# Kernel optimization log

Measured on AMD Instinct MI355X. Metric: run time of the kernel, lower is better.

The kernel has to match this reference:

```python
import jax, jax.numpy as jnp
import numpy as np

DIM, HEADS, DEPTH, SEQ, LOCAL_W = 1024, 16, 7, 2048, 64
HEAD_DIM = DIM // HEADS
SCALE = 1.0 / HEAD_DIM ** 0.5


def cantor_mask(S, depth, local_window):
    """Allowed (i,j): |i-j| within local window, OR |i-j| lies in the Cantor set
    under `depth` levels of ternary subdivision (no base-3 digit equals 1)."""
    idx = np.arange(S)
    d = np.abs(idx[:, None] - idx[None, :])
    x = d.copy()
    ok = np.ones_like(d, dtype=bool)
    for _ in range(depth):
        ok &= (x % 3) != 1
        x //= 3
    ok &= x == 0  # offset must be < 3**depth
    return jnp.asarray(ok | (d <= local_window))  # [S, S] bool


def setup_inputs() -> dict:
    key = jax.random.key(0)
    ks = jax.random.split(key, 8)
    B = 2
    s = 0.02
    return {
        "query": jax.random.normal(ks[0], (B, SEQ, DIM), jnp.float32),
        "key_value": jax.random.normal(ks[1], (B, SEQ, DIM), jnp.float32),
        "Wq": jax.random.normal(ks[2], (DIM, DIM), jnp.float32) * s,
        "bq": jnp.zeros((DIM,), jnp.float32),
        "Wkv": jax.random.normal(ks[3], (DIM, 2 * DIM), jnp.float32) * s,
        "bkv": jnp.zeros((2 * DIM,), jnp.float32),
        "Wo": jax.random.normal(ks[4], (DIM, DIM), jnp.float32) * s,
        "bo": jnp.zeros((DIM,), jnp.float32),
    }


def reference(query, key_value, Wq, bq, Wkv, bkv, Wo, bo):
    B, S, D = query.shape
    H, hd = HEADS, HEAD_DIM
    mask = cantor_mask(S, DEPTH, LOCAL_W)  # static [S, S] bool

    q = (query @ Wq + bq).reshape(B, S, H, hd).transpose(0, 2, 1, 3)  # [B,H,S,hd]
    kv = (key_value @ Wkv + bkv).reshape(B, S, 2, H, hd).transpose(2, 0, 3, 1, 4)
    k, v = kv[0], kv[1]  # [B,H,S,hd]

    scores = jnp.einsum("bhqd,bhkd->bhqk", q, k) * SCALE
    scores = jnp.where(mask, scores, jnp.finfo(scores.dtype).min)
    attn = jax.nn.softmax(scores, axis=-1)
    out = jnp.einsum("bhqk,bhkd->bhqd", attn, v)  # [B,H,S,hd]
    out = out.transpose(0, 2, 1, 3).reshape(B, S, D)
    return out @ Wo + bo
```

## Files before the change

kernel.cpp:

```cpp
#include <hip/hip_runtime.h>
#include <stdint.h>

typedef _Float16 half_t;
typedef __attribute__((ext_vector_type(8))) _Float16 half8;
typedef __attribute__((ext_vector_type(4))) _Float16 half4;
typedef __attribute__((ext_vector_type(4))) float floatx4;

#define SEQ 2048
#define NH 16
#define HD 64

#define MFMA16(a, b, c) __builtin_amdgcn_mfma_f32_16x16x16f16(a, b, c, 0, 0, 0)
#define MFMA32K(a, b, c) __builtin_amdgcn_mfma_f32_16x16x32_f16(a, b, c, 0, 0, 0)

#define QSCALE 0.1803368801111306f

__global__ __launch_bounds__(256) void prep(
    const float* __restrict__ query, const float* __restrict__ key_value,
    const float* __restrict__ Wq, const float* __restrict__ Wkv,
    const float* __restrict__ Wo, half_t* __restrict__ xq,
    half_t* __restrict__ xkv, half_t* __restrict__ wqT,
    half_t* __restrict__ wkvT, half_t* __restrict__ woT,
    uint8_t* __restrict__ tok, uint8_t* __restrict__ tok16,
    uint64_t* __restrict__ maskw) {
  int bx = blockIdx.x, tid = threadIdx.x;
  if (bx < 2048) {
    const float* s; half_t* d; int base;
    if (bx < 1024) { s = query; d = xq; base = bx * 4096; }
    else { s = key_value; d = xkv; base = (bx - 1024) * 4096; }
#pragma unroll
    for (int u = 0; u < 4; ++u) {
      int i = base + u * 1024 + tid * 4;
      floatx4 v = *(const floatx4*)(s + i);
      half4 h;
      h[0] = (half_t)v[0]; h[1] = (half_t)v[1];
      h[2] = (half_t)v[2]; h[3] = (half_t)v[3];
      *(half4*)(d + i) = h;
    }
    return;
  }
  if (bx < 3072) {
    __shared__ float tile[64][65];
    int id = bx - 2048;
    const float* W; half_t* Wt; int N, nt, kt;
    if (id < 256) { W = Wq; Wt = wqT; N = 1024; nt = id & 15; kt = id >> 4; }
    else if (id < 768) { int i2 = id - 256; W = Wkv; Wt = wkvT; N = 2048; nt = i2 & 31; kt = i2 >> 5; }
    else { int i2 = id - 768; W = Wo; Wt = woT; N = 1024; nt = i2 & 15; kt = i2 >> 4; }
    const int K = 1024;
    int n0 = nt * 64, k0 = kt * 64;
    {
      int rr = tid >> 4, cc = (tid & 15) * 4;
#pragma unroll
      for (int u = 0; u < 4; ++u) {
        floatx4 v = *(const floatx4*)(W + (size_t)(k0 + rr + u * 16) * N + n0 + cc);
        tile[rr + u * 16][cc] = v[0];
        tile[rr + u * 16][cc + 1] = v[1];
        tile[rr + u * 16][cc + 2] = v[2];
        tile[rr + u * 16][cc + 3] = v[3];
      }
    }
    __syncthreads();
    {
      int n = tid >> 2, q4 = tid & 3;
      half_t h[16];
#pragma unroll
      for (int s = 0; s < 16; ++s) h[s] = (half_t)tile[q4 * 16 + s][n];
      half_t* dst = Wt + (size_t)(n0 + n) * K + k0 + q4 * 16;
      *(half8*)dst = *(half8*)&h[0];
      *(half8*)(dst + 8) = *(half8*)&h[8];
    }
    return;
  }
  __shared__ uint8_t slut[2048];
  int ib = bx - 3072;
  for (int d = tid; d < 2048; d += 256) {
    int x = d;
    bool ok = true;
    for (int it = 0; it < 7; ++it) { ok &= ((x % 3) != 1); x /= 3; }
    ok &= (x == 0);
    slut[d] = (ok || d <= 64) ? 1 : 0;
  }
  __syncthreads();
  if (ib == 0) {
    if (tid < 64) {
      int delta = tid - 32;
      int lo = delta * 64 - 63, hi = delta * 64 + 63;
      uint8_t any = 0;
      for (int x = lo; x <= hi; ++x) {
        int a = x < 0 ? -x : x;
        if (a < 2048) any |= slut[a];
      }
      tok[tid] = any;
    }
    {
      int d16 = tid - 128;
      int ctr = d16 * 16;
      uint8_t any = 0;
      for (int x = ctr - 15; x <= ctr + 15; ++x) {
        int a = x < 0 ? -x : x;
        if (a < 2048) any |= slut[a];
      }
      tok16[tid] = any;
    }
  }
  int g = ib * 256 + tid;
  int tt = g - 2048;
  uint64_t w = 0;
  for (int jj = 0; jj < 64; ++jj) {
    int d = tt - jj; d = d < 0 ? -d : d;
    if (d < 2048 && slut[d]) w |= (1ull << jj);
  }
  maskw[g] = w;
}

__device__ __forceinline__ void cp16(half_t* lds, const half_t* g) {
  __builtin_amdgcn_global_load_lds(
      (const __attribute__((address_space(1))) uint32_t*)g,
      (__attribute__((address_space(3))) uint32_t*)lds, 16, 0, 0);
}

__global__ __launch_bounds__(256) void gemm_qkv(
    const half_t* __restrict__ xq, const half_t* __restrict__ xkv,
    const half_t* __restrict__ wqT, const half_t* __restrict__ wkvT,
    const float* __restrict__ bq, const float* __restrict__ bkv,
    half_t* __restrict__ qout, half_t* __restrict__ kout,
    half_t* __restrict__ vTout) {
  extern __shared__ char smemraw[];
  half_t* As = (half_t*)smemraw;
  half_t* Bs = As + 8192;
  const int K = 1024;
  bool isq = blockIdx.y < 8;
  const half_t* A = isq ? xq : xkv;
  const half_t* Bt = isq ? wqT : wkvT;
  const float* bias = isq ? bq : bkv;
  int n0 = (isq ? blockIdx.y : (blockIdx.y - 8)) * 128;
  int m0 = blockIdx.x * 128;

  int tid = threadIdx.x;
  int wave = tid >> 6, lane = tid & 63;
  int c = lane & 15, quad = lane >> 4;
  int wm = (wave >> 1) * 64, wn = (wave & 1) * 64;

  floatx4 acc[4][4] = {};
  int arow = tid >> 2, akc = (tid & 3) * 8;

  cp16(&As[wave * 512], A + (size_t)(m0 + arow) * K + akc);
  cp16(&As[2048 + wave * 512], A + (size_t)(m0 + 64 + arow) * K + akc);
  cp16(&Bs[wave * 512], Bt + (size_t)(n0 + arow) * K + akc);
  cp16(&Bs[2048 + wave * 512], Bt + (size_t)(n0 + 64 + arow) * K + akc);

  for (int kt = 0; kt < 32; ++kt) {
    __syncthreads();
    if (kt + 1 < 32) {
      int k0 = (kt + 1) * 32;
      int b = (kt + 1) & 1;
      cp16(&As[b * 4096 + wave * 512], A + (size_t)(m0 + arow) * K + k0 + akc);
      cp16(&As[b * 4096 + 2048 + wave * 512], A + (size_t)(m0 + 64 + arow) * K + k0 + akc);
      cp16(&Bs[b * 4096 + wave * 512], Bt + (size_t)(n0 + arow) * K + k0 + akc);
      cp16(&Bs[b * 4096 + 2048 + wave * 512], Bt + (size_t)(n0 + 64 + arow) * K + k0 + akc);
    }
    int b = kt & 1;
    half8 af[4], bf[4];
#pragma unroll
    for (int mt = 0; mt < 4; ++mt)
      af[mt] = *(const half8*)&As[b * 4096 + (wm + mt * 16 + c) * 32 + quad * 8];
#pragma unroll
    for (int nt = 0; nt < 4; ++nt)
      bf[nt] = *(const half8*)&Bs[b * 4096 + (wn + nt * 16 + c) * 32 + quad * 8];
#pragma unroll
    for (int mt = 0; mt < 4; ++mt)
#pragma unroll
      for (int nt = 0; nt < 4; ++nt)
        acc[mt][nt] = MFMA32K(af[mt], bf[nt], acc[mt][nt]);
  }

  __syncthreads();
  half_t* ep = (half_t*)smemraw;
  int bb = m0 >> 11, sbase = m0 & 2047;
  bool isv = (!isq) && (n0 >= 1024);

  if (!isv) {
#pragma unroll
    for (int nt = 0; nt < 4; ++nt) {
      int nl = wn + nt * 16 + c;
      float bv = bias[n0 + nl];
#pragma unroll
      for (int mt = 0; mt < 4; ++mt)
#pragma unroll
        for (int r = 0; r < 4; ++r) {
          int ml = wm + mt * 16 + quad * 4 + r;
          float v = acc[mt][nt][r] + bv;
          if (isq) v *= QSCALE;
          ep[ml * 128 + nl] = (half_t)v;
        }
    }
    __syncthreads();
    half_t* outp = isq ? qout : kout;
#pragma unroll
    for (int rd = 0; rd < 8; ++rd) {
      int id = rd * 256 + tid;
      int ml = id >> 4, ch = id & 15;
      int ng = n0 + ch * 8;
      int h = ng >> 6, d0 = ng & 63;
      half8 v = *(const half8*)&ep[ml * 128 + ch * 8];
      *(half8*)(outp + ((size_t)(bb * 16 + h) * SEQ + sbase + ml) * 64 + d0) = v;
    }
  } else {
#pragma unroll
    for (int nt = 0; nt < 4; ++nt) {
      int nl = wn + nt * 16 + c;
      float bv = bias[n0 + nl];
#pragma unroll
      for (int mt = 0; mt < 4; ++mt) {
        int ml = wm + mt * 16 + quad * 4;
        half4 hv;
#pragma unroll
        for (int r = 0; r < 4; ++r) hv[r] = (half_t)(acc[mt][nt][r] + bv);
        *(half4*)&ep[nl * 136 + ml] = hv;
      }
    }
    __syncthreads();
#pragma unroll
    for (int rd = 0; rd < 8; ++rd) {
      int id = rd * 256 + tid;
      int nl = id >> 4, mc = id & 15;
      int ng = n0 + nl;
      int h = (ng >> 6) & 15, d = ng & 63;
      half8 v = *(const half8*)&ep[nl * 136 + mc * 8];
      *(half8*)(vTout + ((size_t)(bb * 16 + h) * 64 + d) * SEQ + sbase + mc * 8) = v;
    }
  }
}

__global__ __launch_bounds__(256) void gemm_out(
    const half_t* __restrict__ A, const half_t* __restrict__ Bt,
    const float* __restrict__ bias, float* __restrict__ outf) {
  __shared__ half_t As[2][128 * 32];
  __shared__ half_t Bs[2][64 * 32];
  const int K = 1024;
  int tid = threadIdx.x;
  int wave = tid >> 6, lane = tid & 63;
  int c = lane & 15, quad = lane >> 4;
  int wm = (wave >> 1) * 64, wn = (wave & 1) * 32;
  int m0 = blockIdx.x * 128, n0 = blockIdx.y * 64;

  floatx4 acc[4][2] = {};
  int arow = tid >> 2, akc = (tid & 3) * 8;

  cp16(&As[0][wave * 512], A + (size_t)(m0 + arow) * K + akc);
  cp16(&As[0][2048 + wave * 512], A + (size_t)(m0 + 64 + arow) * K + akc);
  cp16(&Bs[0][wave * 512], Bt + (size_t)(n0 + arow) * K + akc);

  for (int kt = 0; kt < 32; ++kt) {
    __syncthreads();
    if (kt + 1 < 32) {
      int k0 = (kt + 1) * 32;
      int b = (kt + 1) & 1;
      cp16(&As[b][wave * 512], A + (size_t)(m0 + arow) * K + k0 + akc);
      cp16(&As[b][2048 + wave * 512], A + (size_t)(m0 + 64 + arow) * K + k0 + akc);
      cp16(&Bs[b][wave * 512], Bt + (size_t)(n0 + arow) * K + k0 + akc);
    }
    int b = kt & 1;
    half8 af[4], bf[2];
#pragma unroll
    for (int mt = 0; mt < 4; ++mt)
      af[mt] = *(const half8*)&As[b][(wm + mt * 16 + c) * 32 + quad * 8];
#pragma unroll
    for (int nt = 0; nt < 2; ++nt)
      bf[nt] = *(const half8*)&Bs[b][(wn + nt * 16 + c) * 32 + quad * 8];
#pragma unroll
    for (int mt = 0; mt < 4; ++mt)
#pragma unroll
      for (int nt = 0; nt < 2; ++nt)
        acc[mt][nt] = MFMA32K(af[mt], bf[nt], acc[mt][nt]);
  }

#pragma unroll
  for (int nt = 0; nt < 2; ++nt) {
    int n = n0 + wn + nt * 16 + c;
    float bv = bias[n];
#pragma unroll
    for (int mt = 0; mt < 4; ++mt)
#pragma unroll
      for (int r = 0; r < 4; ++r) {
        int m = m0 + wm + mt * 16 + quad * 4 + r;
        outf[(size_t)m * 1024 + n] = acc[mt][nt][r] + bv;
      }
  }
}

__global__ __launch_bounds__(512) void attn_kernel(
    const half_t* __restrict__ qb, const half_t* __restrict__ kb,
    const half_t* __restrict__ vTg, half_t* __restrict__ ctx,
    const uint64_t* __restrict__ maskw, const uint8_t* __restrict__ tok,
    const uint8_t* __restrict__ tok16g) {
  __shared__ half_t kT[2][64 * 64];
  __shared__ half_t vT[2][64 * 64];
  __shared__ half_t ot[128 * 72];
  __shared__ int list[34];
  __shared__ uint8_t tok16s[256];

  int tid = threadIdx.x, wave = tid >> 6, lane = tid & 63;
  int c = lane & 15, q = lane >> 4;
  int id = blockIdx.x;
  int bh = (id & 7) * 4 + ((id >> 3) & 3);
  int it128 = id >> 5;
  int i0 = it128 << 7;
  const half_t* qbase = qb + (size_t)bh * SEQ * HD;
  const half_t* kg = kb + (size_t)bh * SEQ * HD;
  const half_t* vg = vTg + (size_t)bh * HD * SEQ;

  if (tid < 256) tok16s[tid] = tok16g[tid];
  if (wave == 0) {
    int jt = lane;
    int base = i0 >> 6;
    bool act = (jt < 32) &&
               (tok[(jt - base) + 32] | tok[(jt - base - 1) + 32]);
    unsigned long long bal = __ballot(act);
    if (act) {
      int pre = __popcll(bal & ((1ull << jt) - 1));
      list[1 + pre] = jt << 6;
    }
    if (lane == 0) list[0] = __popcll(bal);
  }

  int i_row = i0 + wave * 16 + c;
  int it16 = (i0 >> 4) + wave;
  half8 qf0 = *(const half8*)(qbase + (size_t)i_row * 64 + q * 8);
  half8 qf1 = *(const half8*)(qbase + (size_t)i_row * 64 + 32 + q * 8);

  floatx4 oacc[4] = {};
  floatx4 lacc = {};
  half4 ones;
  ones[0] = (half_t)1.f; ones[1] = (half_t)1.f;
  ones[2] = (half_t)1.f; ones[3] = (half_t)1.f;

  int srow = tid >> 3;
  int sch = tid & 7;
  int ssw = srow & 7;
  int soff = srow * 64 + ((sch ^ ssw) * 8);

  __syncthreads();
  int nact = list[0];

  {
    int j0 = list[1];
    *(half8*)&kT[0][soff] = *(const half8*)(kg + (size_t)(j0 + srow) * 64 + sch * 8);
    *(half8*)&vT[0][soff] = *(const half8*)(vg + (size_t)srow * SEQ + j0 + sch * 8);
  }
  half8 kr, vr;
  if (nact > 1) {
    int j1 = list[2];
    kr = *(const half8*)(kg + (size_t)(j1 + srow) * 64 + sch * 8);
    vr = *(const half8*)(vg + (size_t)srow * SEQ + j1 + sch * 8);
  }
  __syncthreads();
  int buf = 0;

  for (int ti = 0; ti < nact; ++ti) {
    int jcur = list[1 + ti];
    uint64_t w = maskw[(i_row - jcur) + 2048];
    int bidx = (jcur >> 4) - it16 + 128;
    if (ti + 1 < nact) {
      *(half8*)&kT[buf ^ 1][soff] = kr;
      *(half8*)&vT[buf ^ 1][soff] = vr;
      if (ti + 2 < nact) {
        int j2 = list[3 + ti];
        kr = *(const half8*)(kg + (size_t)(j2 + srow) * 64 + sch * 8);
        vr = *(const half8*)(vg + (size_t)srow * SEQ + j2 + sch * 8);
      }
    }
    const half_t* kTb = &kT[buf][0];
    const half_t* vTb = &vT[buf][0];

    uint32_t wlo = (uint32_t)(w >> (4 * q));
    uint32_t whi = (uint32_t)(w >> (32 + 4 * q));
#pragma unroll
    for (int jt = 0; jt < 4; ++jt) {
      if (!tok16s[bidx + jt]) continue;
      int row = jt * 16 + c;
      int sw = c & 7;
      half8 a0 = *(const half8*)&kTb[row * 64 + ((q ^ sw) * 8)];
      half8 a1 = *(const half8*)&kTb[row * 64 + (((4 + q) ^ sw) * 8)];
      floatx4 t = {};
      t = MFMA32K(a0, qf0, t);
      t = MFMA32K(a1, qf1, t);
      uint32_t ww = (jt < 2) ? wlo : whi;
#pragma unroll
      for (int r = 0; r < 4; ++r) {
        float p = __builtin_exp2f(t[r]);
        int bitpos = 16 * (jt & 1) + r;
        uint32_t msk = (uint32_t)(((int)(ww << (31 - bitpos))) >> 31);
        t[r] = __uint_as_float(__float_as_uint(p) & msk);
      }
      auto lo = __builtin_amdgcn_cvt_pkrtz(t[0], t[1]);
      auto hi = __builtin_amdgcn_cvt_pkrtz(t[2], t[3]);
      half4 pb;
      pb[0] = lo[0]; pb[1] = lo[1]; pb[2] = hi[0]; pb[3] = hi[1];
      lacc = MFMA16(ones, pb, lacc);
#pragma unroll
      for (int mt = 0; mt < 4; ++mt) {
        int drow = mt * 16 + c;
        int ch = 2 * jt + (q >> 1);
        half4 a = *(const half4*)&vTb[drow * 64 + ((ch ^ sw) * 8) + (q & 1) * 4];
        oacc[mt] = MFMA16(a, pb, oacc[mt]);
      }
    }
    __syncthreads();
    buf ^= 1;
  }

  float inv_l = 1.0f / lacc[0];
#pragma unroll
  for (int mt = 0; mt < 4; ++mt)
#pragma unroll
    for (int r = 0; r < 4; ++r)
      ot[(wave * 16 + c) * 72 + mt * 16 + 4 * q + r] = (half_t)(oacc[mt][r] * inv_l);
  __syncthreads();
  {
    int row = tid >> 2, chq = tid & 3;
    int b = bh >> 4, h = bh & 15;
    size_t base = (((size_t)(b * SEQ + i0 + row) * NH) + h) * 64 + chq * 16;
    half8 v0 = *(const half8*)&ot[row * 72 + chq * 16];
    half8 v1 = *(const half8*)&ot[row * 72 + chq * 16 + 8];
    *(half8*)(ctx + base) = v0;
    *(half8*)(ctx + base + 8) = v1;
  }
}

extern "C" void kernel_launch(void* const* d_in, const int* in_sizes, int n_in,
                              void* d_out, int out_size, void* d_ws, size_t ws_size,
                              hipStream_t stream) {
  const float* query = (const float*)d_in[0];
  const float* key_value = (const float*)d_in[1];
  const float* Wq = (const float*)d_in[2];
  const float* bq = (const float*)d_in[3];
  const float* Wkv = (const float*)d_in[4];
  const float* bkv = (const float*)d_in[5];
  const float* Wo = (const float*)d_in[6];
  const float* bo = (const float*)d_in[7];

  char* ws = (char*)d_ws;
  uint8_t* tok = (uint8_t*)ws;
  uint8_t* tok16 = (uint8_t*)(ws + 1024);
  uint64_t* maskw = (uint64_t*)(ws + 4096);
  const size_t MB = 1ull << 20;
  half_t* xq = (half_t*)(ws + 1 * MB);
  half_t* xkv = (half_t*)(ws + 9 * MB);
  half_t* wqT = (half_t*)(ws + 17 * MB);
  half_t* wkvT = (half_t*)(ws + 19 * MB);
  half_t* woT = (half_t*)(ws + 23 * MB);
  half_t* qbuf = (half_t*)(ws + 25 * MB);
  half_t* kbuf = (half_t*)(ws + 33 * MB);
  half_t* vTg = (half_t*)(ws + 41 * MB);
  half_t* ctx = xq;

  hipLaunchKernelGGL(prep, dim3(3088), dim3(256), 0, stream,
                     query, key_value, Wq, Wkv, Wo, xq, xkv, wqT, wkvT, woT,
                     tok, tok16, maskw);
  hipLaunchKernelGGL(gemm_qkv, dim3(32, 24), dim3(256), 34816, stream,
                     xq, xkv, wqT, wkvT, bq, bkv, qbuf, kbuf, vTg);
  hipLaunchKernelGGL(attn_kernel, dim3(512), dim3(512), 0, stream,
                     qbuf, kbuf, vTg, ctx, maskw, tok, tok16);
  hipLaunchKernelGGL(gemm_out, dim3(32, 16), dim3(256), 0, stream,
                     ctx, woT, bo, (float*)d_out);
}
```

Baseline: 216.5 us.

## Use half-precision mask table, stage gemm_out epilogue in LDS, alias attention LDS

The per-offset 64-bit mask words become a table of four half values per offset. The attention inner loop now multiplies the exp2 results by the loaded half4 mask instead of doing bit-shift selects. This removes integer ALU work but adds a small global load per 16-key subtile. Separately, the gemm_out epilogue writes accumulators to shared memory and then stores coalesced float4 rows instead of scattered scalar stores, and the attention kernel's K/V/output LDS buffers are merged into one aliased array to cut its LDS footprint.

After: 212.0 us. -2.1%, faster.

```diff
diff --git a/kernel.cpp b/kernel.cpp
--- a/kernel.cpp
+++ b/kernel.cpp
@@ -22,7 +22,7 @@
     half_t* __restrict__ xkv, half_t* __restrict__ wqT,
     half_t* __restrict__ wkvT, half_t* __restrict__ woT,
     uint8_t* __restrict__ tok, uint8_t* __restrict__ tok16,
-    uint64_t* __restrict__ maskw) {
+    half_t* __restrict__ maskh) {
   int bx = blockIdx.x, tid = threadIdx.x;
   if (bx < 2048) {
     const float* s; half_t* d; int base;
@@ -103,14 +103,17 @@
       tok16[tid] = any;
     }
   }
-  int g = ib * 256 + tid;
-  int tt = g - 2048;
-  uint64_t w = 0;
-  for (int jj = 0; jj < 64; ++jj) {
-    int d = tt - jj; d = d < 0 ? -d : d;
-    if (d < 2048 && slut[d]) w |= (1ull << jj);
-  }
-  maskw[g] = w;
+  {
+    int g = ib * 256 + tid;
+    int t = g - 2048;
+    half4 mh;
+#pragma unroll
+    for (int r = 0; r < 4; ++r) {
+      int d = t - r; d = d < 0 ? -d : d;
+      mh[r] = (half_t)((d < 2048 && slut[d]) ? 1.f : 0.f);
+    }
+    *(half4*)(maskh + (size_t)g * 4) = mh;
+  }
 }
 
 __device__ __forceinline__ void cp16(half_t* lds, const half_t* g) {
@@ -235,8 +238,9 @@
 __global__ __launch_bounds__(256) void gemm_out(
     const half_t* __restrict__ A, const half_t* __restrict__ Bt,
     const float* __restrict__ bias, float* __restrict__ outf) {
-  __shared__ half_t As[2][128 * 32];
-  __shared__ half_t Bs[2][64 * 32];
+  extern __shared__ char smemraw[];
+  half_t* As = (half_t*)smemraw;
+  half_t* Bs = As + 8192;
   const int K = 1024;
   int tid = threadIdx.x;
   int wave = tid >> 6, lane = tid & 63;
@@ -247,27 +251,27 @@
   floatx4 acc[4][2] = {};
   int arow = tid >> 2, akc = (tid & 3) * 8;
 
-  cp16(&As[0][wave * 512], A + (size_t)(m0 + arow) * K + akc);
-  cp16(&As[0][2048 + wave * 512], A + (size_t)(m0 + 64 + arow) * K + akc);
-  cp16(&Bs[0][wave * 512], Bt + (size_t)(n0 + arow) * K + akc);
+  cp16(&As[wave * 512], A + (size_t)(m0 + arow) * K + akc);
+  cp16(&As[2048 + wave * 512], A + (size_t)(m0 + 64 + arow) * K + akc);
+  cp16(&Bs[wave * 512], Bt + (size_t)(n0 + arow) * K + akc);
 
   for (int kt = 0; kt < 32; ++kt) {
     __syncthreads();
     if (kt + 1 < 32) {
       int k0 = (kt + 1) * 32;
       int b = (kt + 1) & 1;
-      cp16(&As[b][wave * 512], A + (size_t)(m0 + arow) * K + k0 + akc);
-      cp16(&As[b][2048 + wave * 512], A + (size_t)(m0 + 64 + arow) * K + k0 + akc);
-      cp16(&Bs[b][wave * 512], Bt + (size_t)(n0 + arow) * K + k0 + akc);
+      cp16(&As[b * 4096 + wave * 512], A + (size_t)(m0 + arow) * K + k0 + akc);
+      cp16(&As[b * 4096 + 2048 + wave * 512], A + (size_t)(m0 + 64 + arow) * K + k0 + akc);
+      cp16(&Bs[b * 2048 + wave * 512], Bt + (size_t)(n0 + arow) * K + k0 + akc);
     }
     int b = kt & 1;
     half8 af[4], bf[2];
 #pragma unroll
     for (int mt = 0; mt < 4; ++mt)
-      af[mt] = *(const half8*)&As[b][(wm + mt * 16 + c) * 32 + quad * 8];
+      af[mt] = *(const half8*)&As[b * 4096 + (wm + mt * 16 + c) * 32 + quad * 8];
 #pragma unroll
     for (int nt = 0; nt < 2; ++nt)
-      bf[nt] = *(const half8*)&Bs[b][(wn + nt * 16 + c) * 32 + quad * 8];
+      bf[nt] = *(const half8*)&Bs[b * 2048 + (wn + nt * 16 + c) * 32 + quad * 8];
 #pragma unroll
     for (int mt = 0; mt < 4; ++mt)
 #pragma unroll
@@ -275,28 +279,36 @@
         acc[mt][nt] = MFMA32K(af[mt], bf[nt], acc[mt][nt]);
   }
 
+  __syncthreads();
+  float* ep = (float*)smemraw;
 #pragma unroll
   for (int nt = 0; nt < 2; ++nt) {
-    int n = n0 + wn + nt * 16 + c;
-    float bv = bias[n];
+    int nl = wn + nt * 16 + c;
+    float bv = bias[n0 + nl];
 #pragma unroll
     for (int mt = 0; mt < 4; ++mt)
 #pragma unroll
       for (int r = 0; r < 4; ++r) {
-        int m = m0 + wm + mt * 16 + quad * 4 + r;
-        outf[(size_t)m * 1024 + n] = acc[mt][nt][r] + bv;
-      }
+        int ml = wm + mt * 16 + quad * 4 + r;
+        ep[ml * 64 + nl] = acc[mt][nt][r] + bv;
+      }
+  }
+  __syncthreads();
+#pragma unroll
+  for (int rd = 0; rd < 8; ++rd) {
+    int id = rd * 256 + tid;
+    int ml = id >> 4, ch = id & 15;
+    floatx4 v = *(const floatx4*)&ep[ml * 64 + ch * 4];
+    *(floatx4*)(outf + (size_t)(m0 + ml) * 1024 + n0 + ch * 4) = v;
   }
 }
 
 __global__ __launch_bounds__(512) void attn_kernel(
     const half_t* __restrict__ qb, const half_t* __restrict__ kb,
     const half_t* __restrict__ vTg, half_t* __restrict__ ctx,
-    const uint64_t* __restrict__ maskw, const uint8_t* __restrict__ tok,
+    const half_t* __restrict__ maskhg, const uint8_t* __restrict__ tok,
     const uint8_t* __restrict__ tok16g) {
-  __shared__ half_t kT[2][64 * 64];
-  __shared__ half_t vT[2][64 * 64];
-  __shared__ half_t ot[128 * 72];
+  __shared__ half_t sm[16384];
   __shared__ int list[34];
   __shared__ uint8_t tok16s[256];
 
@@ -345,8 +357,8 @@
 
   {
     int j0 = list[1];
-    *(half8*)&kT[0][soff] = *(const half8*)(kg + (size_t)(j0 + srow) * 64 + sch * 8);
-    *(half8*)&vT[0][soff] = *(const half8*)(vg + (size_t)srow * SEQ + j0 + sch * 8);
+    *(half8*)&sm[soff] = *(const half8*)(kg + (size_t)(j0 + srow) * 64 + sch * 8);
+    *(half8*)&sm[8192 + soff] = *(const half8*)(vg + (size_t)srow * SEQ + j0 + sch * 8);
   }
   half8 kr, vr;
   if (nact > 1) {
@@ -359,22 +371,20 @@
 
   for (int ti = 0; ti < nact; ++ti) {
     int jcur = list[1 + ti];
-    uint64_t w = maskw[(i_row - jcur) + 2048];
     int bidx = (jcur >> 4) - it16 + 128;
+    int tmbase = i_row - jcur - 4 * q + 2048;
     if (ti + 1 < nact) {
-      *(half8*)&kT[buf ^ 1][soff] = kr;
-      *(half8*)&vT[buf ^ 1][soff] = vr;
+      *(half8*)&sm[(buf ^ 1) * 4096 + soff] = kr;
+      *(half8*)&sm[8192 + (buf ^ 1) * 4096 + soff] = vr;
       if (ti + 2 < nact) {
         int j2 = list[3 + ti];
         kr = *(const half8*)(kg + (size_t)(j2 + srow) * 64 + sch * 8);
         vr = *(const half8*)(vg + (size_t)srow * SEQ + j2 + sch * 8);
       }
     }
-    const half_t* kTb = &kT[buf][0];
-    const half_t* vTb = &vT[buf][0];
-
-    uint32_t wlo = (uint32_t)(w >> (4 * q));
-    uint32_t whi = (uint32_t)(w >> (32 + 4 * q));
+    const half_t* kTb = &sm[buf * 4096];
+    const half_t* vTb = &sm[8192 + buf * 4096];
+
 #pragma unroll
     for (int jt = 0; jt < 4; ++jt) {
       if (!tok16s[bidx + jt]) continue;
@@ -385,18 +395,14 @@
       floatx4 t = {};
       t = MFMA32K(a0, qf0, t);
       t = MFMA32K(a1, qf1, t);
-      uint32_t ww = (jt < 2) ? wlo : whi;
-#pragma unroll
-      for (int r = 0; r < 4; ++r) {
-        float p = __builtin_exp2f(t[r]);
-        int bitpos = 16 * (jt & 1) + r;
-        uint32_t msk = (uint32_t)(((int)(ww << (31 - bitpos))) >> 31);
-        t[r] = __uint_as_float(__float_as_uint(p) & msk);
-      }
-      auto lo = __builtin_amdgcn_cvt_pkrtz(t[0], t[1]);
-      auto hi = __builtin_amdgcn_cvt_pkrtz(t[2], t[3]);
+      half4 mh = *(const half4*)(maskhg + (size_t)(tmbase - jt * 16) * 4);
+      auto lo = __builtin_amdgcn_cvt_pkrtz(__builtin_exp2f(t[0]),
+                                           __builtin_exp2f(t[1]));
+      auto hi = __builtin_amdgcn_cvt_pkrtz(__builtin_exp2f(t[2]),
+                                           __builtin_exp2f(t[3]));
       half4 pb;
       pb[0] = lo[0]; pb[1] = lo[1]; pb[2] = hi[0]; pb[3] = hi[1];
+      pb *= mh;
       lacc = MFMA16(ones, pb, lacc);
 #pragma unroll
       for (int mt = 0; mt < 4; ++mt) {
@@ -410,6 +416,7 @@
     buf ^= 1;
   }
 
+  half_t* ot = &sm[0];
   float inv_l = 1.0f / lacc[0];
 #pragma unroll
   for (int mt = 0; mt < 4; ++mt)
@@ -443,7 +450,7 @@
   char* ws = (char*)d_ws;
   uint8_t* tok = (uint8_t*)ws;
   uint8_t* tok16 = (uint8_t*)(ws + 1024);
-  uint64_t* maskw = (uint64_t*)(ws + 4096);
+  half_t* maskh = (half_t*)(ws + 4096);
   const size_t MB = 1ull << 20;
   half_t* xq = (half_t*)(ws + 1 * MB);
   half_t* xkv = (half_t*)(ws + 9 * MB);
@@ -457,11 +464,11 @@
 
   hipLaunchKernelGGL(prep, dim3(3088), dim3(256), 0, stream,
                      query, key_value, Wq, Wkv, Wo, xq, xkv, wqT, wkvT, woT,
-                     tok, tok16, maskw);
+                     tok, tok16, maskh);
   hipLaunchKernelGGL(gemm_qkv, dim3(32, 24), dim3(256), 34816, stream,
                      xq, xkv, wqT, wkvT, bq, bkv, qbuf, kbuf, vTg);
   hipLaunchKernelGGL(attn_kernel, dim3(512), dim3(512), 0, stream,
-                     qbuf, kbuf, vTg, ctx, maskw, tok, tok16);
-  hipLaunchKernelGGL(gemm_out, dim3(32, 16), dim3(256), 0, stream,
+                     qbuf, kbuf, vTg, ctx, maskh, tok, tok16);
+  hipLaunchKernelGGL(gemm_out, dim3(32, 16), dim3(256), 32768, stream,
                      ctx, woT, bo, (float*)d_out);
 }
```
